# Kernel optimization log

Hardware: AMD Instinct MI355X
Metric: run time of the kernel (lower is better)

The kernel has to match this reference:

```python
import jax, jax.numpy as jnp
import numpy as np

EMBED_DIM = 256
N_HEADS = 1
NORM_FACTOR = float(np.sqrt(EMBED_DIM / N_HEADS))


def setup_inputs() -> dict:
    key = jax.random.key(0)
    ks = jax.random.split(key, 7)
    B, S, E = 4, 4096, EMBED_DIM
    scale = 1.0 / np.sqrt(E)
    x = jax.random.normal(ks[0], (B, S, E), dtype=jnp.float32)
    Wq = jax.random.normal(ks[1], (E, E), dtype=jnp.float32) * scale
    bq = jax.random.normal(ks[2], (E,), dtype=jnp.float32) * 0.01
    Wk = jax.random.normal(ks[3], (E, E), dtype=jnp.float32) * scale
    bk = jax.random.normal(ks[4], (E,), dtype=jnp.float32) * 0.01
    Wv = jax.random.normal(ks[5], (E, E), dtype=jnp.float32) * scale
    bv = jax.random.normal(ks[6], (E,), dtype=jnp.float32) * 0.01
    return {"x": x, "Wq": Wq, "bq": bq, "Wk": Wk, "bk": bk, "Wv": Wv, "bv": bv}


def reference(x, Wq, bq, Wk, bk, Wv, bv):
    # Linear projections (torch Linear: x @ W.T + b; W here stored as [in, out]-equivalent square)
    q = x @ Wq + bq  # [B, S, E]
    k = x @ Wk + bk  # [B, S, E]
    v = x @ Wv + bv  # [B, S, E]
    # Full attention scores [B, S, S], scaled by sqrt(embed_dim / n_heads)
    attn_scores = jnp.einsum('bse,bte->bst', q, k) / NORM_FACTOR
    attn_dist = jax.nn.softmax(attn_scores, axis=-1)
    pooled = jnp.einsum('bst,bte->bse', attn_dist, v)  # [B, S, E]
    return pooled.mean(axis=1, keepdims=True)  # [B, 1, E]
```

## Files before the change

kernel.cpp:

```cpp
#include <hip/hip_runtime.h>
#include <hip/hip_fp8.h>
#include <stdint.h>

#define SS 4096
#define EE 256
#define C2 0.0901684400555602f
#define SCALE1 0x7F7F7F7F
#define ZMAX 8.5f

typedef __bf16 bf16x8 __attribute__((ext_vector_type(8)));
typedef float  f32x4  __attribute__((ext_vector_type(4)));
typedef float  f32x2  __attribute__((ext_vector_type(2)));
typedef int    i32x8  __attribute__((ext_vector_type(8)));

#if __has_builtin(__builtin_amdgcn_exp2f)
#define EXP2(x) __builtin_amdgcn_exp2f(x)
#else
#define EXP2(x) exp2f(x)
#endif
#if __has_builtin(__builtin_amdgcn_rcpf)
#define RCP(x) __builtin_amdgcn_rcpf(x)
#else
#define RCP(x) (1.0f / (x))
#endif

__device__ __forceinline__ uint16_t bf16_rn(float f) {
  uint32_t u = __float_as_uint(f);
  uint32_t r = (u + 0x7fffu + ((u >> 16) & 1u)) >> 16;
  return (uint16_t)r;
}
__device__ __forceinline__ float bf2f(uint16_t h) {
  return __uint_as_float(((uint32_t)h) << 16);
}
__device__ __forceinline__ bf16x8 pack_bf8(float4 a, float4 b) {
  union { bf16x8 v; uint16_t u[8]; } r;
  r.u[0] = bf16_rn(a.x); r.u[1] = bf16_rn(a.y);
  r.u[2] = bf16_rn(a.z); r.u[3] = bf16_rn(a.w);
  r.u[4] = bf16_rn(b.x); r.u[5] = bf16_rn(b.y);
  r.u[6] = bf16_rn(b.z); r.u[7] = bf16_rn(b.w);
  return r.v;
}
__device__ __forceinline__ uint8_t f32_to_e4m3(float x) {
#if __has_builtin(__builtin_amdgcn_cvt_pk_fp8_f32)
  return (uint8_t)(__builtin_amdgcn_cvt_pk_fp8_f32(x, 0.f, 0, false) & 0xff);
#else
  __hip_fp8_e4m3 h(x);
  return (uint8_t)h.__x;
#endif
}
__device__ __forceinline__ uint32_t pack4_e4m3(float a, float b, float c, float d) {
#if __has_builtin(__builtin_amdgcn_cvt_pk_fp8_f32)
  int v = __builtin_amdgcn_cvt_pk_fp8_f32(a, b, 0, false);
  v = __builtin_amdgcn_cvt_pk_fp8_f32(c, d, v, true);
  return (uint32_t)v;
#else
  return (uint32_t)f32_to_e4m3(a) | ((uint32_t)f32_to_e4m3(b) << 8) |
         ((uint32_t)f32_to_e4m3(c) << 16) | ((uint32_t)f32_to_e4m3(d) << 24);
#endif
}
__device__ __forceinline__ float e4m3_f32(uint32_t u) {
  uint32_t bits = ((u & 0x80u) << 24) | ((u & 0x7fu) << 20);
  return __uint_as_float(bits) * 0x1p+120f;
}
__device__ __forceinline__ void decode_fma4(uint32_t w, float rv, float* acc) {
#if __has_builtin(__builtin_amdgcn_cvt_pk_f32_fp8)
  f32x2 lo = __builtin_amdgcn_cvt_pk_f32_fp8((int)w, false);
  f32x2 hi = __builtin_amdgcn_cvt_pk_f32_fp8((int)w, true);
  acc[0] += rv * lo[0]; acc[1] += rv * lo[1];
  acc[2] += rv * hi[0]; acc[3] += rv * hi[1];
#else
  acc[0] += rv * e4m3_f32(w & 0xffu);
  acc[1] += rv * e4m3_f32((w >> 8) & 0xffu);
  acc[2] += rv * e4m3_f32((w >> 16) & 0xffu);
  acc[3] += rv * e4m3_f32(w >> 24);
#endif
}

__device__ __forceinline__ f32x4 mfma16(bf16x8 a, bf16x8 b, f32x4 c) {
  return __builtin_amdgcn_mfma_f32_16x16x32_bf16(a, b, c, 0, 0, 0);
}
__device__ __forceinline__ f32x4 mfma128(i32x8 a, i32x8 b, f32x4 c) {
  return __builtin_amdgcn_mfma_scale_f32_16x16x128_f8f6f4(
      a, b, c, 0 , 0 , 0, SCALE1, 0, SCALE1);
}

template<int R>
__device__ __forceinline__ void stage_tile(const uint16_t* gsrc, char* lds, int tid) {
  constexpr int NPER = (R * 32) / 256;
  const int wave = tid >> 6;
  #pragma unroll
  for (int c = 0; c < NPER; ++c) {
    int chunk = c * 256 + tid;
    int r = chunk >> 5;
    int ccl = (chunk & 31) ^ (r & 31);
    const char* gp = (const char*)gsrc + (r * 32 + ccl) * 16;
    char* lp = lds + (c * 256 + wave * 64) * 16;
    __builtin_amdgcn_global_load_lds(
        (const __attribute__((address_space(1))) uint32_t*)(uintptr_t)gp,
        (__attribute__((address_space(3))) uint32_t*)(uintptr_t)lp,
        16, 0, 0);
  }
}
__device__ __forceinline__ bf16x8 read_frag(const char* lds, int row, int cc) {
  int ccp = cc ^ (row & 31);
  return *(const bf16x8*)(lds + (row * 32 + ccp) * 16);
}

__device__ __forceinline__ void stage_fp8_64(const uint8_t* gsrc, char* lds, int tid) {
  #pragma unroll
  for (int c = 0; c < 4; ++c) {
    int chunk = c * 256 + tid;
    int r = chunk >> 4;
    int ccl = (chunk & 15) ^ (r & 15);
    const char* gp = (const char*)gsrc + (r * 16 + ccl) * 16;
    char* lp = lds + (c * 256 + (tid >> 6) * 64) * 16;
    __builtin_amdgcn_global_load_lds(
        (const __attribute__((address_space(1))) uint32_t*)(uintptr_t)gp,
        (__attribute__((address_space(3))) uint32_t*)(uintptr_t)lp,
        16, 0, 0);
  }
}
__device__ __forceinline__ i32x8 read_frag8(const char* lds, int t, int win, int quad) {
  union { i32x8 v; uint4 q[2]; } r;
  int cc0 = win * 8 + quad * 2;
  r.q[0] = *(const uint4*)(lds + (t * 16 + ((cc0 + 0) ^ (t & 15))) * 16);
  r.q[1] = *(const uint4*)(lds + (t * 16 + ((cc0 + 1) ^ (t & 15))) * 16);
  return r.v;
}

__global__ void prep_kernel(const float* __restrict__ Wq, const float* __restrict__ Wk,
                            const float* __restrict__ Wv, uint16_t* __restrict__ wt,
                            float* __restrict__ zbase, float* __restrict__ out) {
  __shared__ float t[64][65];
  const int bid = blockIdx.x, tid = threadIdx.x;
  if (bid >= 48) {
    int idx = (bid - 48) * 256 + tid;
    float4 z = {0.f, 0.f, 0.f, 0.f};
    if (idx < 8192) ((float4*)zbase)[idx] = z;
    else ((float4*)out)[idx - 8192] = z;
    return;
  }
  const int mat = bid >> 4, tt = bid & 15;
  const int ib = (tt >> 2) * 64, ob = (tt & 3) * 64;
  const float* W = (mat == 0) ? Wq : (mat == 1) ? Wk : Wv;
  #pragma unroll
  for (int p = 0; p < 4; ++p) {
    int idx = p * 256 + tid;
    int r = idx >> 4, c4 = idx & 15;
    float4 f = *(const float4*)&W[(size_t)(ib + r) * 256 + ob + c4 * 4];
    t[r][c4 * 4 + 0] = f.x; t[r][c4 * 4 + 1] = f.y;
    t[r][c4 * 4 + 2] = f.z; t[r][c4 * 4 + 3] = f.w;
  }
  __syncthreads();
  #pragma unroll
  for (int p = 0; p < 4; ++p) {
    int idx = p * 256 + tid;
    int o = idx >> 4, i4 = idx & 15;
    ushort4 u;
    u.x = bf16_rn(t[i4 * 4 + 0][o]);
    u.y = bf16_rn(t[i4 * 4 + 1][o]);
    u.z = bf16_rn(t[i4 * 4 + 2][o]);
    u.w = bf16_rn(t[i4 * 4 + 3][o]);
    *(ushort4*)&wt[((size_t)mat * 256 + ob + o) * 256 + ib + i4 * 4] = u;
  }
}

__global__ __launch_bounds__(256, 2) void qkv_kernel(
    const float* __restrict__ x, const uint16_t* __restrict__ wt,
    const float* __restrict__ bq, const float* __restrict__ bk, const float* __restrict__ bv,
    uint8_t* __restrict__ q8, uint8_t* __restrict__ k8, uint16_t* __restrict__ vo) {
  __shared__ char wsm[2][32768];
  const int tid = threadIdx.x;
  const int lane = tid & 63, wave = tid >> 6, quad = lane >> 4, lr = lane & 15;
  const int m0 = (blockIdx.x >> 2) * 128;
  const int cchunk = blockIdx.x & 3;
  stage_tile<64>(wt + (size_t)(cchunk * 192) * 256, wsm[0], tid);
  const float* ab = x + (size_t)(m0 + wave * 32) * EE;
  bf16x8 a[2][8];
  #pragma unroll
  for (int ms = 0; ms < 2; ++ms)
    #pragma unroll
    for (int f = 0; f < 8; ++f) {
      const float* rp = ab + (size_t)(ms * 16 + lr) * EE + f * 32 + quad * 8;
      a[ms][f] = pack_bf8(*(const float4*)rp, *(const float4*)(rp + 4));
    }
  for (int nc = 0; nc < 3; ++nc) {
    __syncthreads();
    if (nc < 2)
      stage_tile<64>(wt + (size_t)(cchunk * 192 + (nc + 1) * 64) * 256, wsm[(nc + 1) & 1], tid);
    const char* tile = wsm[nc & 1];
    #pragma unroll
    for (int nt = 0; nt < 4; ++nt) {
      const int eg0 = cchunk * 192 + nc * 64 + nt * 16;
      const int mat = eg0 >> 8;
      const int e = (eg0 & 255) + lr;
      const float* bias = (mat == 0) ? bq : (mat == 1) ? bk : bv;
      bf16x8 bf[8];
      #pragma unroll
      for (int f = 0; f < 8; ++f) bf[f] = read_frag(tile, nt * 16 + lr, f * 4 + quad);
      f32x4 acc[2] = {};
      #pragma unroll
      for (int f = 0; f < 8; ++f)
        #pragma unroll
        for (int ms = 0; ms < 2; ++ms)
          acc[ms] = mfma16(a[ms][f], bf[f], acc[ms]);
      const float bsv = bias[e];
      #pragma unroll
      for (int ms = 0; ms < 2; ++ms)
        #pragma unroll
        for (int r = 0; r < 4; ++r) {
          int row = m0 + wave * 32 + ms * 16 + quad * 4 + r;
          float vl = acc[ms][r] + bsv;
          if (mat == 2)      vo[(size_t)row * EE + e] = bf16_rn(vl);
          else if (mat == 1) k8[(size_t)row * EE + e] = f32_to_e4m3(vl);
          else               q8[(size_t)row * EE + e] = f32_to_e4m3(vl);
        }
    }
  }
}

__global__ __launch_bounds__(256, 2) void scores_pl_kernel(
    const uint8_t* __restrict__ q8, const uint8_t* __restrict__ k8,
    uint8_t* __restrict__ p8, float* __restrict__ lacc) {
  __shared__ char kt[4][16384];
  __shared__ float lsh[256];
  const int tid = threadIdx.x;
  const int lane = tid & 63, wave = tid >> 6, quad = lane >> 4, lr = lane & 15;
  const int idx = blockIdx.x;
  const int b = idx >> 8, rem = idx & 255, kblk = rem >> 4, sch = rem & 15;
  const uint8_t* kb0 = k8 + (size_t)(b * SS + kblk * 256) * EE;
  const uint8_t* qw = q8 + (size_t)(b * SS + sch * 256) * EE;
  lsh[tid] = 0.f;
  #pragma unroll
  for (int w = 0; w < 4; ++w)
    stage_fp8_64(kb0 + (size_t)w * 64 * EE, kt[w], tid);
  const char* myt = kt[wave];
  const size_t chunkbase = ((size_t)((b * 16 + sch) * 16 + kblk)) << 16;
  uint8_t* pst = p8 + chunkbase + (size_t)(wave * 16) * 1024 + (size_t)lane * 16;
  __syncthreads();
  #pragma unroll
  for (int it = 0; it < 4; ++it) {
    #pragma unroll
    for (int nt = 0; nt < 4; ++nt) {
      const uint8_t* qrow = qw + (size_t)(it * 64 + nt * 16 + lr) * EE;
      i32x8 bf0 = *(const i32x8*)(qrow + quad * 32);
      i32x8 bf1 = *(const i32x8*)(qrow + 128 + quad * 32);
      f32x4 acc[4] = {};
      #pragma unroll
      for (int ms = 0; ms < 4; ++ms) {
        acc[ms] = mfma128(read_frag8(myt, ms * 16 + lr, 0, quad), bf0, acc[ms]);
        acc[ms] = mfma128(read_frag8(myt, ms * 16 + lr, 1, quad), bf1, acc[ms]);
      }
      const int sloc = it * 64 + nt * 16 + lr;
      float lpart = 0.f;
      uint32_t pw[4];
      #pragma unroll
      for (int ms = 0; ms < 4; ++ms) {
        float e0 = EXP2(fminf(acc[ms][0] * C2, ZMAX));
        float e1 = EXP2(fminf(acc[ms][1] * C2, ZMAX));
        float e2 = EXP2(fminf(acc[ms][2] * C2, ZMAX));
        float e3 = EXP2(fminf(acc[ms][3] * C2, ZMAX));
        lpart += (e0 + e1) + (e2 + e3);
        pw[ms] = pack4_e4m3(e0, e1, e2, e3);
      }
      uint4 w4; w4.x = pw[0]; w4.y = pw[1]; w4.z = pw[2]; w4.w = pw[3];
      *(uint4*)(pst + (size_t)(it * 4 + nt) * 1024) = w4;
      lpart += __shfl_xor(lpart, 16, 64);
      lpart += __shfl_xor(lpart, 32, 64);
      if (quad == 0) atomicAdd(&lsh[sloc], lpart);
    }
  }
  __syncthreads();
  atomicAdd(&lacc[b * SS + sch * 256 + tid], lsh[tid]);
}

__global__ __launch_bounds__(256) void wsum_kernel(
    const uint8_t* __restrict__ p8, const float* __restrict__ lacc,
    float* __restrict__ wacc) {
  __shared__ float rls[256];
  const int tid = threadIdx.x;
  const int idx = blockIdx.x;
  const int b = idx >> 9;
  const int sch = (idx >> 5) & 15;
  const int kblk = (idx >> 1) & 15;
  const int half = idx & 1;
  rls[tid] = RCP(lacc[b * SS + sch * 256 + tid]);
  __syncthreads();
  const int lane = tid & 63, wave_w = tid >> 6, lr = tid & 15;
  const size_t chunkbase = ((size_t)((b * 16 + sch) * 16 + kblk)) << 16;
  const uint8_t* pp = p8 + chunkbase +
      (size_t)(wave_w * 16 + half * 8) * 1024 + (size_t)lane * 16;
  float acc[16];
  #pragma unroll
  for (int i = 0; i < 16; ++i) acc[i] = 0.f;
  #pragma unroll
  for (int i = 0; i < 8; ++i) {
    const int itnt = half * 8 + i;
    uint4 pv = *(const uint4*)(pp + (size_t)i * 1024);
    float rv = rls[(itnt >> 2) * 64 + (itnt & 3) * 16 + lr];
    decode_fma4(pv.x, rv, acc + 0);
    decode_fma4(pv.y, rv, acc + 4);
    decode_fma4(pv.z, rv, acc + 8);
    decode_fma4(pv.w, rv, acc + 12);
  }
  #pragma unroll
  for (int d = 1; d < 16; d <<= 1)
    #pragma unroll
    for (int i = 0; i < 16; ++i)
      acc[i] += __shfl_xor(acc[i], d, 64);
  if (lr == 0) {
    float* wp = wacc + b * SS + kblk * 256 + wave_w * 64 + (lane >> 4) * 4;
    #pragma unroll
    for (int ms = 0; ms < 4; ++ms)
      #pragma unroll
      for (int r = 0; r < 4; ++r)
        atomicAdd(&wp[ms * 16 + r], acc[ms * 4 + r]);
  }
}

__global__ void pool_kernel(const float* __restrict__ wvec, const uint16_t* __restrict__ v,
                            float* __restrict__ out) {
  __shared__ float red[4][256];
  const int b = blockIdx.x >> 6, tc = blockIdx.x & 63;
  const int tq = threadIdx.x >> 6, eg = threadIdx.x & 63;
  float acc[4] = {0.f, 0.f, 0.f, 0.f};
  const float* wp = wvec + b * SS + tc * 64;
  const uint16_t* vp = v + (size_t)(b * SS + tc * 64) * EE + eg * 4;
  #pragma unroll
  for (int t = 0; t < 16; ++t) {
    int row = t * 4 + tq;
    float wv = wp[row];
    ushort4 x4 = *(const ushort4*)(vp + (size_t)row * EE);
    acc[0] += wv * bf2f(x4.x);
    acc[1] += wv * bf2f(x4.y);
    acc[2] += wv * bf2f(x4.z);
    acc[3] += wv * bf2f(x4.w);
  }
  #pragma unroll
  for (int j = 0; j < 4; ++j) red[tq][eg * 4 + j] = acc[j];
  __syncthreads();
  if (tq == 0) {
    const float inv = 1.0f / 4096.0f;
    #pragma unroll
    for (int j = 0; j < 4; ++j) {
      float s = red[0][eg * 4 + j] + red[1][eg * 4 + j] +
                red[2][eg * 4 + j] + red[3][eg * 4 + j];
      atomicAdd(&out[b * 256 + eg * 4 + j], s * inv);
    }
  }
}

extern "C" void kernel_launch(void* const* d_in, const int* in_sizes, int n_in,
                              void* d_out, int out_size, void* d_ws, size_t ws_size,
                              hipStream_t stream) {
  const float* x  = (const float*)d_in[0];
  const float* Wq = (const float*)d_in[1];
  const float* bq = (const float*)d_in[2];
  const float* Wk = (const float*)d_in[3];
  const float* bk = (const float*)d_in[4];
  const float* Wv = (const float*)d_in[5];
  const float* bv = (const float*)d_in[6];

  char* ws = (char*)d_ws;
  uint8_t*  q8    = (uint8_t*)(ws);
  uint8_t*  k8    = (uint8_t*)(ws + 4194304);
  uint16_t* vb    = (uint16_t*)(ws + 8388608);
  uint16_t* wt    = (uint16_t*)(ws + 16777216);
  float*    l_arr = (float*)(ws + 17170432);
  float*    w_arr = (float*)(ws + 17235968);
  uint8_t*  p8    = (uint8_t*)(ws + 33554432);
  float* out      = (float*)d_out;

  prep_kernel<<<81, 256, 0, stream>>>(Wq, Wk, Wv, wt, l_arr, out);
  qkv_kernel<<<512, 256, 0, stream>>>(x, wt, bq, bk, bv, q8, k8, vb);
  scores_pl_kernel<<<1024, 256, 0, stream>>>(q8, k8, p8, l_arr);
  wsum_kernel<<<2048, 256, 0, stream>>>(p8, l_arr, w_arr);
  pool_kernel<<<256, 256, 0, stream>>>(w_arr, vb, out);
}
```

Before: 165.0 us.

## Shrink score tiles to 64 keys per block for higher occupancy

The scores kernel now stages a single 64-row fp8 K tile (16 KB LDS instead of 64 KB) and each wave handles 64 query rows against it. Launch bounds rise to 6 blocks per SM and the grid grows fourfold. The wsum kernel is remapped to the new P chunk layout and reduces across waves in shared memory before one atomic per key, replacing the per-lane global atomics. This trades more blocks, more K/Q reloads from L2 and more lacc atomics for better occupancy and latency hiding.

Result: faster. 158.7 us (-3.8%).

```diff
diff --git a/kernel.cpp b/kernel.cpp
--- a/kernel.cpp
+++ b/kernel.cpp
@@ -219,56 +219,48 @@
   }
 }
 
-__global__ __launch_bounds__(256, 2) void scores_pl_kernel(
+__global__ __launch_bounds__(256, 6) void scores_pl_kernel(
     const uint8_t* __restrict__ q8, const uint8_t* __restrict__ k8,
     uint8_t* __restrict__ p8, float* __restrict__ lacc) {
-  __shared__ char kt[4][16384];
+  __shared__ char kt[16384];
   __shared__ float lsh[256];
   const int tid = threadIdx.x;
   const int lane = tid & 63, wave = tid >> 6, quad = lane >> 4, lr = lane & 15;
   const int idx = blockIdx.x;
-  const int b = idx >> 8, rem = idx & 255, kblk = rem >> 4, sch = rem & 15;
-  const uint8_t* kb0 = k8 + (size_t)(b * SS + kblk * 256) * EE;
-  const uint8_t* qw = q8 + (size_t)(b * SS + sch * 256) * EE;
-  lsh[tid] = 0.f;
-  #pragma unroll
-  for (int w = 0; w < 4; ++w)
-    stage_fp8_64(kb0 + (size_t)w * 64 * EE, kt[w], tid);
-  const char* myt = kt[wave];
-  const size_t chunkbase = ((size_t)((b * 16 + sch) * 16 + kblk)) << 16;
-  uint8_t* pst = p8 + chunkbase + (size_t)(wave * 16) * 1024 + (size_t)lane * 16;
+  const int b = idx >> 10, rem = idx & 1023, sch = rem >> 6, kblk = rem & 63;
+  const uint8_t* kb0 = k8 + (size_t)(b * SS + kblk * 64) * EE;
+  const uint8_t* qw  = q8 + (size_t)(b * SS + sch * 256 + wave * 64) * EE;
+  stage_fp8_64(kb0, kt, tid);
+  const size_t chunkbase = ((size_t)((b * 16 + sch) * 64 + kblk)) << 14;
+  uint8_t* pst = p8 + chunkbase + (size_t)(wave * 4) * 1024 + (size_t)lane * 16;
   __syncthreads();
   #pragma unroll
   for (int it = 0; it < 4; ++it) {
-    #pragma unroll
-    for (int nt = 0; nt < 4; ++nt) {
-      const uint8_t* qrow = qw + (size_t)(it * 64 + nt * 16 + lr) * EE;
-      i32x8 bf0 = *(const i32x8*)(qrow + quad * 32);
-      i32x8 bf1 = *(const i32x8*)(qrow + 128 + quad * 32);
-      f32x4 acc[4] = {};
-      #pragma unroll
-      for (int ms = 0; ms < 4; ++ms) {
-        acc[ms] = mfma128(read_frag8(myt, ms * 16 + lr, 0, quad), bf0, acc[ms]);
-        acc[ms] = mfma128(read_frag8(myt, ms * 16 + lr, 1, quad), bf1, acc[ms]);
-      }
-      const int sloc = it * 64 + nt * 16 + lr;
-      float lpart = 0.f;
-      uint32_t pw[4];
-      #pragma unroll
-      for (int ms = 0; ms < 4; ++ms) {
-        float e0 = EXP2(fminf(acc[ms][0] * C2, ZMAX));
-        float e1 = EXP2(fminf(acc[ms][1] * C2, ZMAX));
-        float e2 = EXP2(fminf(acc[ms][2] * C2, ZMAX));
-        float e3 = EXP2(fminf(acc[ms][3] * C2, ZMAX));
-        lpart += (e0 + e1) + (e2 + e3);
-        pw[ms] = pack4_e4m3(e0, e1, e2, e3);
-      }
-      uint4 w4; w4.x = pw[0]; w4.y = pw[1]; w4.z = pw[2]; w4.w = pw[3];
-      *(uint4*)(pst + (size_t)(it * 4 + nt) * 1024) = w4;
-      lpart += __shfl_xor(lpart, 16, 64);
-      lpart += __shfl_xor(lpart, 32, 64);
-      if (quad == 0) atomicAdd(&lsh[sloc], lpart);
-    }
+    const uint8_t* qrow = qw + (size_t)(it * 16 + lr) * EE;
+    i32x8 bf0 = *(const i32x8*)(qrow + quad * 32);
+    i32x8 bf1 = *(const i32x8*)(qrow + 128 + quad * 32);
+    f32x4 acc[4] = {};
+    #pragma unroll
+    for (int ms = 0; ms < 4; ++ms) {
+      acc[ms] = mfma128(read_frag8(kt, ms * 16 + lr, 0, quad), bf0, acc[ms]);
+      acc[ms] = mfma128(read_frag8(kt, ms * 16 + lr, 1, quad), bf1, acc[ms]);
+    }
+    float lpart = 0.f;
+    uint32_t pw[4];
+    #pragma unroll
+    for (int ms = 0; ms < 4; ++ms) {
+      float e0 = EXP2(fminf(acc[ms][0] * C2, ZMAX));
+      float e1 = EXP2(fminf(acc[ms][1] * C2, ZMAX));
+      float e2 = EXP2(fminf(acc[ms][2] * C2, ZMAX));
+      float e3 = EXP2(fminf(acc[ms][3] * C2, ZMAX));
+      lpart += (e0 + e1) + (e2 + e3);
+      pw[ms] = pack4_e4m3(e0, e1, e2, e3);
+    }
+    uint4 w4; w4.x = pw[0]; w4.y = pw[1]; w4.z = pw[2]; w4.w = pw[3];
+    *(uint4*)(pst + (size_t)it * 1024) = w4;
+    lpart += __shfl_xor(lpart, 16, 64);
+    lpart += __shfl_xor(lpart, 32, 64);
+    if (quad == 0) lsh[wave * 64 + it * 16 + lr] = lpart;
   }
   __syncthreads();
   atomicAdd(&lacc[b * SS + sch * 256 + tid], lsh[tid]);
@@ -278,26 +270,22 @@
     const uint8_t* __restrict__ p8, const float* __restrict__ lacc,
     float* __restrict__ wacc) {
   __shared__ float rls[256];
+  __shared__ float wred[4][64];
   const int tid = threadIdx.x;
   const int idx = blockIdx.x;
-  const int b = idx >> 9;
-  const int sch = (idx >> 5) & 15;
-  const int kblk = (idx >> 1) & 15;
-  const int half = idx & 1;
+  const int b = idx >> 10, rem = idx & 1023, sch = rem >> 6, kblk = rem & 63;
   rls[tid] = RCP(lacc[b * SS + sch * 256 + tid]);
   __syncthreads();
-  const int lane = tid & 63, wave_w = tid >> 6, lr = tid & 15;
-  const size_t chunkbase = ((size_t)((b * 16 + sch) * 16 + kblk)) << 16;
-  const uint8_t* pp = p8 + chunkbase +
-      (size_t)(wave_w * 16 + half * 8) * 1024 + (size_t)lane * 16;
+  const int lane = tid & 63, w2 = tid >> 6, lr = tid & 15, quad = lane >> 4;
+  const size_t chunkbase = ((size_t)((b * 16 + sch) * 64 + kblk)) << 14;
+  const uint8_t* pp = p8 + chunkbase + (size_t)(w2 * 4) * 1024 + (size_t)lane * 16;
   float acc[16];
   #pragma unroll
   for (int i = 0; i < 16; ++i) acc[i] = 0.f;
   #pragma unroll
-  for (int i = 0; i < 8; ++i) {
-    const int itnt = half * 8 + i;
-    uint4 pv = *(const uint4*)(pp + (size_t)i * 1024);
-    float rv = rls[(itnt >> 2) * 64 + (itnt & 3) * 16 + lr];
+  for (int it = 0; it < 4; ++it) {
+    uint4 pv = *(const uint4*)(pp + (size_t)it * 1024);
+    float rv = rls[w2 * 64 + it * 16 + lr];
     decode_fma4(pv.x, rv, acc + 0);
     decode_fma4(pv.y, rv, acc + 4);
     decode_fma4(pv.z, rv, acc + 8);
@@ -309,13 +297,16 @@
     for (int i = 0; i < 16; ++i)
       acc[i] += __shfl_xor(acc[i], d, 64);
   if (lr == 0) {
-    float* wp = wacc + b * SS + kblk * 256 + wave_w * 64 + (lane >> 4) * 4;
     #pragma unroll
     for (int ms = 0; ms < 4; ++ms)
       #pragma unroll
       for (int r = 0; r < 4; ++r)
-        atomicAdd(&wp[ms * 16 + r], acc[ms * 4 + r]);
-  }
+        wred[w2][ms * 16 + quad * 4 + r] = acc[ms * 4 + r];
+  }
+  __syncthreads();
+  if (tid < 64)
+    atomicAdd(&wacc[b * SS + kblk * 64 + tid],
+              wred[0][tid] + wred[1][tid] + wred[2][tid] + wred[3][tid]);
 }
 
 __global__ void pool_kernel(const float* __restrict__ wvec, const uint16_t* __restrict__ v,
@@ -373,7 +364,7 @@
 
   prep_kernel<<<81, 256, 0, stream>>>(Wq, Wk, Wv, wt, l_arr, out);
   qkv_kernel<<<512, 256, 0, stream>>>(x, wt, bq, bk, bv, q8, k8, vb);
-  scores_pl_kernel<<<1024, 256, 0, stream>>>(q8, k8, p8, l_arr);
-  wsum_kernel<<<2048, 256, 0, stream>>>(p8, l_arr, w_arr);
+  scores_pl_kernel<<<4096, 256, 0, stream>>>(q8, k8, p8, l_arr);
+  wsum_kernel<<<4096, 256, 0, stream>>>(p8, l_arr, w_arr);
   pool_kernel<<<256, 256, 0, stream>>>(w_arr, vb, out);
 }
```
